# Kernel tuning notes

Hardware: AMD Instinct MI355X
Metric: run time of the kernel (lower is better)

The kernel has to match this reference:

```python
import jax, jax.numpy as jnp
import numpy as np

TOPK = 13
ALPHA = 1.0
BETA = 6.0
NUM_CLASSES = 80
NUM_ANCHORS = 100000
NUM_GT = 512
EPS = 1e-9


def _make_boxes(key, n):
    k1, k2 = jax.random.split(key)
    lt = jax.random.uniform(k1, (n, 2)) * 0.5          # x1, y1 in [0, 0.5)
    wh = jax.random.uniform(k2, (n, 2)) * 0.5 + 1e-3   # positive width/height
    return jnp.concatenate([lt, lt + wh], axis=-1)      # [n, 4] valid xyxy


def setup_inputs() -> dict:
    key = jax.random.key(0)
    k1, k2, k3, k4 = jax.random.split(key, 4)
    pd_scores = jax.random.uniform(k1, (NUM_ANCHORS, NUM_CLASSES), dtype=jnp.float32)
    pd_bboxes = _make_boxes(k2, NUM_ANCHORS)
    gt_labels = jax.random.randint(k3, (NUM_GT, 1), 0, NUM_CLASSES, dtype=jnp.int64)
    gt_bboxes = _make_boxes(k4, NUM_GT)
    return {"pd_scores": pd_scores, "pd_bboxes": pd_bboxes,
            "gt_labels": gt_labels, "gt_bboxes": gt_bboxes}


def box_iou(a, b):
    # a: [G, 4], b: [A, 4] in xyxy -> iou [G, A]
    lt = jnp.maximum(a[:, None, :2], b[None, :, :2])
    rb = jnp.minimum(a[:, None, 2:], b[None, :, 2:])
    wh = jnp.clip(rb - lt, 0.0)
    inter = wh[..., 0] * wh[..., 1]                      # [G, A]
    area_a = (a[:, 2] - a[:, 0]) * (a[:, 3] - a[:, 1])   # [G]
    area_b = (b[:, 2] - b[:, 0]) * (b[:, 3] - b[:, 1])   # [A]
    union = area_a[:, None] + area_b[None, :] - inter
    return inter / (union + EPS)


def select_topk_candidates(metrics, topk):
    # metrics: [G, A] -> bool mask [G, A] of per-row topk entries
    _, topk_idx = jax.lax.top_k(metrics, topk)           # [G, topk]
    rows = jnp.arange(metrics.shape[0])[:, None]
    mask = jnp.zeros(metrics.shape, dtype=bool)
    return mask.at[rows, topk_idx].set(True)


def reference(pd_scores, pd_bboxes, gt_labels, gt_bboxes):
    labels = gt_labels.reshape(-1)                       # [G]
    ious = box_iou(gt_bboxes, pd_bboxes)                 # [G, A]
    scores = pd_scores[:, labels].T                      # [G, A] gather by gt class
    metrics = (scores ** ALPHA) * (ious ** BETA)         # alignment metric [G, A]
    is_in_topk = select_topk_candidates(metrics, TOPK)   # [G, A] bool
    max_metrics = jnp.max(metrics, axis=0)               # [A]
    max_indices = jnp.argmax(metrics, axis=0)            # [A]
    target_labels = labels[max_indices]                  # [A]
    target_labels = jnp.where(max_metrics <= 0, NUM_CLASSES, target_labels)
    target_bboxes = gt_bboxes[max_indices]               # [A, 4]
    # is_in_topk is computed (as in the original) and returned so the topk/scatter
    return target_labels, target_bboxes, max_metrics, is_in_topk
```

## Files before the change

kernel.cpp:

```cpp
#include <hip/hip_runtime.h>
#include <cfloat>
#include <cstdint>

#define AN 100000
#define GN 512
#define NC 80
#define KK 13

#define CHUNKS 8
#define CH_LEN 12544
#define DUMP 16
#define GSLICE 8
#define GPS (GN / GSLICE)

typedef unsigned long long ull;

__device__ __forceinline__ float rcpf(float x)
{
    float r; asm("v_rcp_f32 %0, %1" : "=v"(r) : "v"(x)); return r;
}

__device__ __forceinline__ float iou6r(float4 g, float ga, float4 p)
{
    float pa = (p.z - p.x) * (p.w - p.y);
    float ltx = fmaxf(g.x, p.x), lty = fmaxf(g.y, p.y);
    float rbx = fminf(g.z, p.z), rby = fminf(g.w, p.w);
    float w = fmaxf(rbx - ltx, 0.0f), h = fmaxf(rby - lty, 0.0f);
    float inter = w * h;
    float uni = ga + pa - inter;
    float iou = inter * rcpf(uni + 1e-9f);
    float i2 = iou * iou;
    return i2 * i2 * i2;
}

__device__ __forceinline__ unsigned f2ord(float f)
{
    unsigned b = __float_as_uint(f);
    return b ^ (unsigned)(((int)b >> 31) | 0x80000000);
}
__device__ __forceinline__ float ord2f(unsigned u)
{
    unsigned b = (u & 0x80000000u) ? (u ^ 0x80000000u) : ~u;
    return __uint_as_float(b);
}

__device__ __forceinline__ void csw(float& va, int& ia, float& vb, int& ib)
{
    bool sw = (va < vb) || (va == vb && ia > ib);
    float tv = sw ? vb : va; int ti = sw ? ib : ia;
    vb = sw ? va : vb; ib = sw ? ia : ib;
    va = tv; ia = ti;
}

__device__ __forceinline__ void wsync()
{
    __builtin_amdgcn_sched_barrier(0);
    asm volatile("s_waitcnt lgkmcnt(0)" ::: "memory");
    __builtin_amdgcn_sched_barrier(0);
}

__device__ float flush_x(int lane, int n, const float* cand_v, const int* cand_i,
                         const float* __restrict__ srow,
                         float& inc_v, int& inc_i)
{
    wsync();
    float v[8]; int ix[8];
    #pragma unroll
    for (int k = 0; k < 8; ++k) {
        int j = lane + (k << 6);
        bool ok = j < n;
        float i6 = ok ? cand_v[j] : 0.0f;
        int   ai = ok ? cand_i[j] : 0;
        float sc = srow[ai];
        v[k]  = ok ? sc * i6 : -FLT_MAX;
        ix[k] = ok ? ai : 0x7fffffff;
    }
    csw(v[0],ix[0],v[1],ix[1]); csw(v[2],ix[2],v[3],ix[3]);
    csw(v[4],ix[4],v[5],ix[5]); csw(v[6],ix[6],v[7],ix[7]);
    csw(v[0],ix[0],v[2],ix[2]); csw(v[1],ix[1],v[3],ix[3]);
    csw(v[4],ix[4],v[6],ix[6]); csw(v[5],ix[5],v[7],ix[7]);
    csw(v[1],ix[1],v[2],ix[2]); csw(v[5],ix[5],v[6],ix[6]);
    csw(v[0],ix[0],v[4],ix[4]); csw(v[1],ix[1],v[5],ix[5]);
    csw(v[2],ix[2],v[6],ix[6]); csw(v[3],ix[3],v[7],ix[7]);
    csw(v[2],ix[2],v[4],ix[4]); csw(v[3],ix[3],v[5],ix[5]);
    csw(v[1],ix[1],v[2],ix[2]); csw(v[3],ix[3],v[4],ix[4]);
    csw(v[5],ix[5],v[6],ix[6]);
    bool c[8];
    #pragma unroll
    for (int j = 0; j < 8; ++j)
        c[j] = (v[j] > inc_v) || (v[j] == inc_v && ix[j] < inc_i);
    float h[9]; int hi[9];
    h[0] = c[0] ? v[0] : inc_v;  hi[0] = c[0] ? ix[0] : inc_i;
    #pragma unroll
    for (int j = 1; j < 8; ++j) {
        h[j]  = c[j] ? v[j]  : (c[j-1] ? inc_v : v[j-1]);
        hi[j] = c[j] ? ix[j] : (c[j-1] ? inc_i : ix[j-1]);
    }
    h[8] = c[7] ? inc_v : v[7];  hi[8] = c[7] ? inc_i : ix[7];

    float th = -FLT_MAX;
    #pragma unroll
    for (int r = 0; r < KK; ++r) {
        ull myp = ((ull)f2ord(h[0]) << 32) | (unsigned)(~hi[0]);
        ull p = myp;
        #pragma unroll
        for (int o = 32; o >= 1; o >>= 1) {
            ull q = __shfl_xor(p, o);
            p = p > q ? p : q;
        }
        float wv = ord2f((unsigned)(p >> 32));
        int   wi = (int)~((unsigned)p);
        if (lane == r) { inc_v = wv; inc_i = wi; }
        bool pop = (myp == p);
        #pragma unroll
        for (int j = 0; j < 8; ++j) {
            h[j]  = pop ? h[j+1]  : h[j];
            hi[j] = pop ? hi[j+1] : hi[j];
        }
        h[8]  = pop ? -FLT_MAX   : h[8];
        hi[8] = pop ? 0x7fffffff : hi[8];
        th = wv;
    }
    return th;
}

__device__ __forceinline__ void insert13(float* v, int* ix, float m, int a)
{
    bool worse = (m < v[KK - 1]) || (m == v[KK - 1] && a > ix[KK - 1]);
    if (worse) return;
    int p = 0;
    #pragma unroll
    for (int j = 0; j < KK; ++j)
        p += ((v[j] > m) || (v[j] == m && ix[j] < a)) ? 1 : 0;
    #pragma unroll
    for (int j = KK - 1; j >= 1; --j) {
        bool sh = (j > p);
        v[j]  = sh ? v[j - 1]  : v[j];
        ix[j] = sh ? ix[j - 1] : ix[j];
    }
    #pragma unroll
    for (int j = 0; j < KK; ++j) if (j == p) { v[j] = m; ix[j] = a; }
}

__global__ __launch_bounds__(256) void transpose_scores(
    const float* __restrict__ ps, float* __restrict__ scT)
{
    __shared__ float tile[64][NC + 1];
    int a0 = blockIdx.x * 64;
    int tid = threadIdx.x;
    for (int i = tid; i < 64 * NC / 4; i += 256) {
        int fi = i * 4;
        int a = fi / NC, c = fi % NC;
        if (a0 + a < AN) {
            float4 v = *reinterpret_cast<const float4*>(ps + (size_t)(a0 + a) * NC + c);
            tile[a][c] = v.x; tile[a][c + 1] = v.y; tile[a][c + 2] = v.z; tile[a][c + 3] = v.w;
        }
    }
    __syncthreads();
    int j = tid & 63, cg = tid >> 6;
    int a = a0 + j;
    if (a < AN) {
        for (int c = cg; c < NC; c += 4)
            scT[(size_t)c * AN + a] = tile[j][c];
    }
}

__global__ __launch_bounds__(256) void argmax_part(
    const float* __restrict__ pd_bboxes,
    const int*   __restrict__ gt_labels,
    const float* __restrict__ gt_bboxes,
    const float* __restrict__ scT,
    ull* __restrict__ part)
{
    __shared__ float4 gb[GPS];
    __shared__ float  ga[GPS];
    __shared__ int    glb[GPS];
    int slice = blockIdx.x & (GSLICE - 1);
    int ab = (blockIdx.x >> 3) * 512;
    int tid = threadIdx.x;
    int g0 = slice * GPS;
    if (tid < GPS) {
        float4 bb = ((const float4*)gt_bboxes)[g0 + tid];
        gb[tid] = bb;
        ga[tid] = (bb.z - bb.x) * (bb.w - bb.y);
        glb[tid] = gt_labels[g0 + tid];
    }
    __syncthreads();
    int aa = ab + tid, ab2 = ab + 256 + tid;
    bool okA = aa < AN, okB = ab2 < AN;
    int ca = okA ? aa : AN - 1, cb = okB ? ab2 : AN - 1;
    float4 pba = ((const float4*)pd_bboxes)[ca];
    float4 pbb = ((const float4*)pd_bboxes)[cb];
    float bestA = -1.0f, bestB = -1.0f;
    int bgA = 0, bgB = 0;
    for (int i = 0; i < GPS; ++i) {
        float4 gx = gb[i];
        float gax = ga[i];
        int lab = glb[i];
        const float* srow = scT + (size_t)lab * AN;
        float i6a = iou6r(gx, gax, pba);
        float i6b = iou6r(gx, gax, pbb);
        float sa = (i6a > bestA) ? srow[ca] : 0.0f;
        float sb = (i6b > bestB) ? srow[cb] : 0.0f;
        float ma = sa * i6a;
        float mb = sb * i6b;
        if (ma > bestA) { bestA = ma; bgA = i; }
        if (mb > bestB) { bestB = mb; bgB = i; }
    }
    if (okA)
        part[(size_t)slice * AN + aa] =
            ((ull)__float_as_uint(bestA) << 32) | (ull)(0xFFFFFFFFu - (unsigned)(g0 + bgA));
    if (okB)
        part[(size_t)slice * AN + ab2] =
            ((ull)__float_as_uint(bestB) << 32) | (ull)(0xFFFFFFFFu - (unsigned)(g0 + bgB));
}

__global__ __launch_bounds__(256) void argmax_combine(
    const ull* __restrict__ part,
    const int* __restrict__ gt_labels,
    const float* __restrict__ gt_bboxes,
    float* __restrict__ out)
{
    int a = blockIdx.x * 256 + threadIdx.x;
    if (a >= AN) return;
    ull p = part[a];
    #pragma unroll
    for (int s = 1; s < GSLICE; ++s) {
        ull q = part[(size_t)s * AN + a];
        p = p > q ? p : q;
    }
    unsigned g = 0xFFFFFFFFu - (unsigned)(p & 0xFFFFFFFFull);
    float best = __uint_as_float((unsigned)(p >> 32));
    out[a] = (best <= 0.0f) ? (float)NC : (float)gt_labels[g];
    ((float4*)(out + AN))[a] = ((const float4*)gt_bboxes)[g];
    out[(size_t)5 * AN + a] = best;
}

__device__ __forceinline__ void loadB(int tb, int lane,
    const float4* __restrict__ pd4,
    float4& B0, float4& B1, float4& B2, float4& B3)
{
    int a0 = tb + lane;
    B0 = pd4[min(a0,       AN - 1)];
    B1 = pd4[min(a0 + 64,  AN - 1)];
    B2 = pd4[min(a0 + 128, AN - 1)];
    B3 = pd4[min(a0 + 192, AN - 1)];
}

__device__ __forceinline__ void procB(
    int tb, int aend, int lane, uint64_t lt,
    float4 B0, float4 B1, float4 B2, float4 B3,
    const float* __restrict__ srow,
    float4 b, float gax, float& th, int& cnt,
    float* cand_v, int* cand_i, float& inc_v, int& inc_i)
{
    int a0 = tb + lane, a1 = a0 + 64, a2 = a0 + 128, a3 = a0 + 192;
    float i60 = iou6r(b, gax, B0);
    float i61 = iou6r(b, gax, B1);
    float i62 = iou6r(b, gax, B2);
    float i63 = iou6r(b, gax, B3);
    bool h0 = (i60 > th) && (a0 < aend);
    bool h1 = (i61 > th) && (a1 < aend);
    bool h2 = (i62 > th) && (a2 < aend);
    bool h3 = (i63 > th) && (a3 < aend);
    if (__any(h0 | h1 | h2 | h3)) {
        uint64_t B;
        B = __ballot(h0);
        if (h0) { int p = cnt + __popcll(B & lt); cand_v[p] = i60; cand_i[p] = a0; }
        cnt += __popcll(B);
        B = __ballot(h1);
        if (h1) { int p = cnt + __popcll(B & lt); cand_v[p] = i61; cand_i[p] = a1; }
        cnt += __popcll(B);
        B = __ballot(h2);
        if (h2) { int p = cnt + __popcll(B & lt); cand_v[p] = i62; cand_i[p] = a2; }
        cnt += __popcll(B);
        B = __ballot(h3);
        if (h3) { int p = cnt + __popcll(B & lt); cand_v[p] = i63; cand_i[p] = a3; }
        cnt += __popcll(B);
        if (cnt >= 256) {
            th = flush_x(lane, cnt, cand_v, cand_i, srow, inc_v, inc_i);
            cnt = 0;
        }
    }
}

__global__ __launch_bounds__(256, 4) void topk_pass1(
    const float* __restrict__ pd_bboxes,
    const int*   __restrict__ gt_labels,
    const float* __restrict__ gt_bboxes,
    const float* __restrict__ scT,
    float* __restrict__ out_v, int* __restrict__ out_i)
{
    __shared__ float cvA[4][512];
    __shared__ int   ciA[4][512];
    int w = threadIdx.x >> 6, lane = threadIdx.x & 63;
    float* cand_v = cvA[w]; int* cand_i = ciA[w];
    uint64_t lt = (1ull << lane) - 1ull;
    int gid = blockIdx.x * 4 + w;
    int g = gid & (GN - 1), c = gid >> 9;

    float4 b = ((const float4*)gt_bboxes)[g];
    float gax = (b.z - b.x) * (b.w - b.y);
    int lab = gt_labels[g];
    const float* srow = scT + (size_t)lab * AN;
    const float4* pd4 = (const float4*)pd_bboxes;

    int base = c * CH_LEN;
    int len = min(CH_LEN, AN - base);
    int aend = base + len;
    int NT = (len + 255) >> 8;

    float th = -FLT_MAX; int cnt = 0;
    float inc_v = -FLT_MAX; int inc_i = 0x7fffffff;

    float4 X0, X1, X2, X3, Y0, Y1, Y2, Y3;
    loadB(base, lane, pd4, X0, X1, X2, X3);
    int i = 0, tb = base;
    while (true) {
        if (i + 1 < NT) loadB(tb + 256, lane, pd4, Y0, Y1, Y2, Y3);
        procB(tb, aend, lane, lt, X0, X1, X2, X3, srow,
              b, gax, th, cnt, cand_v, cand_i, inc_v, inc_i);
        ++i; tb += 256;
        if (i >= NT) break;
        if (i + 1 < NT) loadB(tb + 256, lane, pd4, X0, X1, X2, X3);
        procB(tb, aend, lane, lt, Y0, Y1, Y2, Y3, srow,
              b, gax, th, cnt, cand_v, cand_i, inc_v, inc_i);
        ++i; tb += 256;
        if (i >= NT) break;
    }

    if (cnt > 0)
        flush_x(lane, cnt, cand_v, cand_i, srow, inc_v, inc_i);

    if (lane < DUMP) {
        size_t o = ((size_t)g * CHUNKS + c) * DUMP + lane;
        out_v[o] = (lane < KK) ? inc_v : -FLT_MAX;
        out_i[o] = (lane < KK) ? inc_i : 0x7fffffff;
    }
}

__global__ __launch_bounds__(256) void topk_finalize(
    const float* __restrict__ in_v, const int* __restrict__ in_i,
    float* __restrict__ mask)
{
    int g = blockIdx.x, tid = threadIdx.x;
    float4* row4 = (float4*)(mask + (size_t)g * AN);
    float4 z = make_float4(0.f, 0.f, 0.f, 0.f);
    for (int j = tid; j < AN / 4; j += 256) row4[j] = z;
    __syncthreads();
    if (tid >= 64) return;
    int lane = tid;
    size_t rb = (size_t)g * (CHUNKS * DUMP);
    float v0 = in_v[rb + lane], v1 = in_v[rb + 64 + lane];
    int   i0 = in_i[rb + lane], i1 = in_i[rb + 64 + lane];
    csw(v0, i0, v1, i1);
    #pragma unroll
    for (int r = 0; r < KK; ++r) {
        ull myp = ((ull)f2ord(v0) << 32) | (unsigned)(~i0);
        ull p = myp;
        #pragma unroll
        for (int o = 32; o >= 1; o >>= 1) {
            ull q = __shfl_xor(p, o);
            p = p > q ? p : q;
        }
        int wi = (int)~((unsigned)p);
        if (lane == r) mask[(size_t)g * AN + wi] = 1.0f;
        bool pop = (myp == p);
        v0 = pop ? v1 : v0;          i0 = pop ? i1 : i0;
        v1 = pop ? -FLT_MAX : v1;    i1 = pop ? 0x7fffffff : i1;
    }
}

__global__ __launch_bounds__(256) void argmax_kernel(
    const float* __restrict__ pd_scores,
    const float* __restrict__ pd_bboxes,
    const int*   __restrict__ gt_labels,
    const float* __restrict__ gt_bboxes,
    const float* __restrict__ scT, int use_t,
    float* __restrict__ out)
{
    __shared__ float4 gb[GN];
    __shared__ float  ga[GN];
    __shared__ int    gl[GN];
    int tid = threadIdx.x;
    for (int g = tid; g < GN; g += 256) {
        float4 b = reinterpret_cast<const float4*>(gt_bboxes)[g];
        gb[g] = b;
        ga[g] = (b.z - b.x) * (b.w - b.y);
        gl[g] = gt_labels[g];
    }
    __syncthreads();
    int a = blockIdx.x * 256 + tid;
    if (a >= AN) return;
    float4 pb = reinterpret_cast<const float4*>(pd_bboxes)[a];
    float best = -1.0f; int bg = 0;
    for (int g = 0; g < GN; ++g) {
        int lab = gl[g];
        float sc = use_t ? scT[(size_t)lab * AN + a] : pd_scores[(size_t)a * NC + lab];
        float m = sc * iou6r(gb[g], ga[g], pb);
        if (m > best) { best = m; bg = g; }
    }
    out[a] = (best <= 0.0f) ? (float)NC : (float)gl[bg];
    reinterpret_cast<float4*>(out + AN)[a] = gb[bg];
    out[5 * AN + a] = best;
}

__global__ __launch_bounds__(256) void topk_kernel_fallback(
    const float* __restrict__ pd_scores,
    const float* __restrict__ pd_bboxes,
    const int*   __restrict__ gt_labels,
    const float* __restrict__ gt_bboxes,
    const float* __restrict__ scT, int use_t,
    float* __restrict__ mask)
{
    __shared__ float sv[256 * KK];
    __shared__ int   si[256 * KK];
    int g = blockIdx.x, tid = threadIdx.x;
    float4 b = reinterpret_cast<const float4*>(gt_bboxes)[g];
    float gax = (b.z - b.x) * (b.w - b.y);
    int lab = gt_labels[g];
    float v[KK]; int idx[KK];
    #pragma unroll
    for (int j = 0; j < KK; ++j) { v[j] = -FLT_MAX; idx[j] = 0x7fffffff; }
    for (int a = tid; a < AN; a += 256) {
        float4 pb = reinterpret_cast<const float4*>(pd_bboxes)[a];
        float sc = use_t ? scT[(size_t)lab * AN + a] : pd_scores[(size_t)a * NC + lab];
        float m = sc * iou6r(b, gax, pb);
        insert13(v, idx, m, a);
    }
    #pragma unroll
    for (int j = 0; j < KK; ++j) { sv[tid * KK + j] = v[j]; si[tid * KK + j] = idx[j]; }
    for (int off = 128; off >= 1; off >>= 1) {
        __syncthreads();
        if (tid < off) {
            int i = 0, jj = 0;
            float ov[KK]; int oi[KK];
            #pragma unroll
            for (int t = 0; t < KK; ++t) {
                float va = sv[tid * KK + i];          int ia = si[tid * KK + i];
                float vb = sv[(tid + off) * KK + jj]; int ib = si[(tid + off) * KK + jj];
                bool ta = (va > vb) || (va == vb && ia < ib);
                ov[t] = ta ? va : vb; oi[t] = ta ? ia : ib;
                i += ta ? 1 : 0; jj += ta ? 0 : 1;
            }
            #pragma unroll
            for (int t = 0; t < KK; ++t) { sv[tid * KK + t] = ov[t]; si[tid * KK + t] = oi[t]; }
        }
    }
    __syncthreads();
    if (tid < KK) mask[(size_t)g * AN + si[tid]] = 1.0f;
}

extern "C" void kernel_launch(void* const* d_in, const int* in_sizes, int n_in,
                              void* d_out, int out_size, void* d_ws, size_t ws_size,
                              hipStream_t stream)
{
    const float* pd_scores = (const float*)d_in[0];
    const float* pd_bboxes = (const float*)d_in[1];
    const int*   gt_labels = (const int*)d_in[2];
    const float* gt_bboxes = (const float*)d_in[3];
    float* out  = (float*)d_out;
    float* mask = out + (size_t)6 * AN;

    const size_t scT_b  = (size_t)NC * AN * sizeof(float);
    const size_t auxn   = (size_t)GN * CHUNKS * DUMP;
    const size_t aux_b  = auxn * 8;
    const size_t part_b = (size_t)GSLICE * AN * sizeof(ull);

    float* scT   = (float*)d_ws;
    float* aux_v = (float*)((char*)d_ws + scT_b);
    int*   aux_i = (int*)(aux_v + auxn);
    ull*   part  = (ull*)((char*)d_ws + scT_b + aux_b);

    if (ws_size >= scT_b + aux_b + part_b) {
        transpose_scores<<<(AN + 63) / 64, 256, 0, stream>>>(pd_scores, scT);
        topk_pass1<<<GN * CHUNKS / 4, 256, 0, stream>>>(
            pd_bboxes, gt_labels, gt_bboxes, scT, aux_v, aux_i);
        topk_finalize<<<GN, 256, 0, stream>>>(aux_v, aux_i, mask);
        argmax_part<<<((AN + 511) / 512) * GSLICE, 256, 0, stream>>>(
            pd_bboxes, gt_labels, gt_bboxes, scT, part);
        argmax_combine<<<(AN + 255) / 256, 256, 0, stream>>>(
            part, gt_labels, gt_bboxes, out);
    } else if (ws_size >= scT_b + aux_b) {
        transpose_scores<<<(AN + 63) / 64, 256, 0, stream>>>(pd_scores, scT);
        topk_pass1<<<GN * CHUNKS / 4, 256, 0, stream>>>(
            pd_bboxes, gt_labels, gt_bboxes, scT, aux_v, aux_i);
        topk_finalize<<<GN, 256, 0, stream>>>(aux_v, aux_i, mask);
        argmax_kernel<<<(AN + 255) / 256, 256, 0, stream>>>(
            pd_scores, pd_bboxes, gt_labels, gt_bboxes, scT, 1, out);
    } else if (ws_size >= scT_b) {
        hipMemsetAsync(mask, 0, (size_t)GN * AN * sizeof(float), stream);
        transpose_scores<<<(AN + 63) / 64, 256, 0, stream>>>(pd_scores, scT);
        argmax_kernel<<<(AN + 255) / 256, 256, 0, stream>>>(
            pd_scores, pd_bboxes, gt_labels, gt_bboxes, scT, 1, out);
        topk_kernel_fallback<<<GN, 256, 0, stream>>>(
            pd_scores, pd_bboxes, gt_labels, gt_bboxes, scT, 1, mask);
    } else {
        hipMemsetAsync(mask, 0, (size_t)GN * AN * sizeof(float), stream);
        argmax_kernel<<<(AN + 255) / 256, 256, 0, stream>>>(
            pd_scores, pd_bboxes, gt_labels, gt_bboxes, scT, 0, out);
        topk_kernel_fallback<<<GN, 256, 0, stream>>>(
            pd_scores, pd_bboxes, gt_labels, gt_bboxes, scT, 0, mask);
    }
}
```

Baseline: 179.4 us.

## Split anchor range into more chunks and peel the bounds-checked tail tile

The top-k first pass now splits the anchors into 16 chunks instead of 8, doubling the number of wavefronts working per GT row. It also raises the occupancy hint in the launch bounds. Full 256-anchor tiles now run without clamped loads or range checks, and only a separate remainder tile keeps them. The finalize kernel merges four candidates per lane, using a small sorting network, instead of two. In exchange, each chunk sees fewer elements before its threshold rises, so there may be more candidate flushes, and the finalize step does more merge work per lane.

```diff
diff --git a/kernel.cpp b/kernel.cpp
--- a/kernel.cpp
+++ b/kernel.cpp
@@ -7,8 +7,8 @@
 #define NC 80
 #define KK 13
 
-#define CHUNKS 8
-#define CH_LEN 12544
+#define CHUNKS 16
+#define CH_LEN 6400
 #define DUMP 16
 #define GSLICE 8
 #define GPS (GN / GSLICE)
@@ -236,17 +236,23 @@
     out[(size_t)5 * AN + a] = best;
 }
 
+template<bool FULL>
 __device__ __forceinline__ void loadB(int tb, int lane,
     const float4* __restrict__ pd4,
     float4& B0, float4& B1, float4& B2, float4& B3)
 {
     int a0 = tb + lane;
-    B0 = pd4[min(a0,       AN - 1)];
-    B1 = pd4[min(a0 + 64,  AN - 1)];
-    B2 = pd4[min(a0 + 128, AN - 1)];
-    B3 = pd4[min(a0 + 192, AN - 1)];
-}
-
+    if (FULL) {
+        B0 = pd4[a0]; B1 = pd4[a0 + 64]; B2 = pd4[a0 + 128]; B3 = pd4[a0 + 192];
+    } else {
+        B0 = pd4[min(a0,       AN - 1)];
+        B1 = pd4[min(a0 + 64,  AN - 1)];
+        B2 = pd4[min(a0 + 128, AN - 1)];
+        B3 = pd4[min(a0 + 192, AN - 1)];
+    }
+}
+
+template<bool FULL>
 __device__ __forceinline__ void procB(
     int tb, int aend, int lane, uint64_t lt,
     float4 B0, float4 B1, float4 B2, float4 B3,
@@ -259,10 +265,10 @@
     float i61 = iou6r(b, gax, B1);
     float i62 = iou6r(b, gax, B2);
     float i63 = iou6r(b, gax, B3);
-    bool h0 = (i60 > th) && (a0 < aend);
-    bool h1 = (i61 > th) && (a1 < aend);
-    bool h2 = (i62 > th) && (a2 < aend);
-    bool h3 = (i63 > th) && (a3 < aend);
+    bool h0 = (i60 > th) && (FULL || a0 < aend);
+    bool h1 = (i61 > th) && (FULL || a1 < aend);
+    bool h2 = (i62 > th) && (FULL || a2 < aend);
+    bool h3 = (i63 > th) && (FULL || a3 < aend);
     if (__any(h0 | h1 | h2 | h3)) {
         uint64_t B;
         B = __ballot(h0);
@@ -284,7 +290,7 @@
     }
 }
 
-__global__ __launch_bounds__(256, 4) void topk_pass1(
+__global__ __launch_bounds__(256, 8) void topk_pass1(
     const float* __restrict__ pd_bboxes,
     const int*   __restrict__ gt_labels,
     const float* __restrict__ gt_bboxes,
@@ -308,25 +314,31 @@
     int base = c * CH_LEN;
     int len = min(CH_LEN, AN - base);
     int aend = base + len;
-    int NT = (len + 255) >> 8;
+    int nfull = len >> 8;
+    int rem = len & 255;
 
     float th = -FLT_MAX; int cnt = 0;
     float inc_v = -FLT_MAX; int inc_i = 0x7fffffff;
 
     float4 X0, X1, X2, X3, Y0, Y1, Y2, Y3;
-    loadB(base, lane, pd4, X0, X1, X2, X3);
+    loadB<true>(base, lane, pd4, X0, X1, X2, X3);
     int i = 0, tb = base;
     while (true) {
-        if (i + 1 < NT) loadB(tb + 256, lane, pd4, Y0, Y1, Y2, Y3);
-        procB(tb, aend, lane, lt, X0, X1, X2, X3, srow,
-              b, gax, th, cnt, cand_v, cand_i, inc_v, inc_i);
+        if (i + 1 < nfull) loadB<true>(tb + 256, lane, pd4, Y0, Y1, Y2, Y3);
+        procB<true>(tb, aend, lane, lt, X0, X1, X2, X3, srow,
+                    b, gax, th, cnt, cand_v, cand_i, inc_v, inc_i);
         ++i; tb += 256;
-        if (i >= NT) break;
-        if (i + 1 < NT) loadB(tb + 256, lane, pd4, X0, X1, X2, X3);
-        procB(tb, aend, lane, lt, Y0, Y1, Y2, Y3, srow,
-              b, gax, th, cnt, cand_v, cand_i, inc_v, inc_i);
+        if (i >= nfull) break;
+        if (i + 1 < nfull) loadB<true>(tb + 256, lane, pd4, X0, X1, X2, X3);
+        procB<true>(tb, aend, lane, lt, Y0, Y1, Y2, Y3, srow,
+                    b, gax, th, cnt, cand_v, cand_i, inc_v, inc_i);
         ++i; tb += 256;
-        if (i >= NT) break;
+        if (i >= nfull) break;
+    }
+    if (rem) {
+        loadB<false>(tb, lane, pd4, X0, X1, X2, X3);
+        procB<false>(tb, aend, lane, lt, X0, X1, X2, X3, srow,
+                     b, gax, th, cnt, cand_v, cand_i, inc_v, inc_i);
     }
 
     if (cnt > 0)
@@ -351,9 +363,13 @@
     if (tid >= 64) return;
     int lane = tid;
     size_t rb = (size_t)g * (CHUNKS * DUMP);
-    float v0 = in_v[rb + lane], v1 = in_v[rb + 64 + lane];
-    int   i0 = in_i[rb + lane], i1 = in_i[rb + 64 + lane];
-    csw(v0, i0, v1, i1);
+    float v0 = in_v[rb + lane],       v1 = in_v[rb + 64 + lane];
+    float v2 = in_v[rb + 128 + lane], v3 = in_v[rb + 192 + lane];
+    int   i0 = in_i[rb + lane],       i1 = in_i[rb + 64 + lane];
+    int   i2 = in_i[rb + 128 + lane], i3 = in_i[rb + 192 + lane];
+    csw(v0, i0, v1, i1); csw(v2, i2, v3, i3);
+    csw(v0, i0, v2, i2); csw(v1, i1, v3, i3);
+    csw(v1, i1, v2, i2);
     #pragma unroll
     for (int r = 0; r < KK; ++r) {
         ull myp = ((ull)f2ord(v0) << 32) | (unsigned)(~i0);
@@ -366,8 +382,10 @@
         int wi = (int)~((unsigned)p);
         if (lane == r) mask[(size_t)g * AN + wi] = 1.0f;
         bool pop = (myp == p);
-        v0 = pop ? v1 : v0;          i0 = pop ? i1 : i0;
-        v1 = pop ? -FLT_MAX : v1;    i1 = pop ? 0x7fffffff : i1;
+        v0 = pop ? v1 : v0;  i0 = pop ? i1 : i0;
+        v1 = pop ? v2 : v1;  i1 = pop ? i2 : i1;
+        v2 = pop ? v3 : v2;  i2 = pop ? i3 : i2;
+        v3 = pop ? -FLT_MAX : v3;  i3 = pop ? 0x7fffffff : i3;
     }
 }
 
```

Result: slower. 370.9 us (+106.7%).

## Process two GT rows per wavefront and prune with division-free IoU threshold

Applied to the files above, without the earlier changes.

The top-k first pass now has each wavefront handle two ground-truth boxes, so every anchor box loaded is reused for two IoU evaluations. The candidate filter compares intersection against a sixth-root threshold times the union, which removes the reciprocal and power from the hot loop; the exact metric is computed only when candidates are flushed. The chunk count doubles to 16 with half the chunk length and an earlier flush threshold, and finalize merges four candidates per lane instead of two. It also removes one fallback launch path and risks edge cases from the approximate root threshold and higher register pressure.

```diff
diff --git a/kernel.cpp b/kernel.cpp
--- a/kernel.cpp
+++ b/kernel.cpp
@@ -7,8 +7,8 @@
 #define NC 80
 #define KK 13
 
-#define CHUNKS 8
-#define CH_LEN 12544
+#define CHUNKS 16
+#define CH_LEN 6400
 #define DUMP 16
 #define GSLICE 8
 #define GPS (GN / GSLICE)
@@ -18,6 +18,11 @@
 __device__ __forceinline__ float rcpf(float x)
 {
     float r; asm("v_rcp_f32 %0, %1" : "=v"(r) : "v"(x)); return r;
+}
+
+__device__ __forceinline__ float root6_down(float th)
+{
+    return exp2f(log2f(th) * (1.0f / 6.0f)) * 0.9999f;
 }
 
 __device__ __forceinline__ float iou6r(float4 g, float ga, float4 p)
@@ -33,6 +38,16 @@
     return i2 * i2 * i2;
 }
 
+__device__ __forceinline__ void iou_iu(float4 g, float gax, float4 p, float pa,
+                                       float& in, float& ue)
+{
+    float lx = fmaxf(g.x, p.x), ly = fmaxf(g.y, p.y);
+    float rx = fminf(g.z, p.z), ry = fminf(g.w, p.w);
+    float w = fmaxf(rx - lx, 0.0f), h = fmaxf(ry - ly, 0.0f);
+    in = w * h;
+    ue = gax + pa - in + 1e-9f;
+}
+
 __device__ __forceinline__ unsigned f2ord(float f)
 {
     unsigned b = __float_as_uint(f);
@@ -59,7 +74,8 @@
     __builtin_amdgcn_sched_barrier(0);
 }
 
-__device__ float flush_x(int lane, int n, const float* cand_v, const int* cand_i,
+__device__ float flush_f(int lane, int n,
+                         const float* c_in, const float* c_ue, const int* c_ix,
                          const float* __restrict__ srow,
                          float& inc_v, int& inc_i)
 {
@@ -67,10 +83,14 @@
     float v[8]; int ix[8];
     #pragma unroll
     for (int k = 0; k < 8; ++k) {
-        int j = lane + (k << 6);
-        bool ok = j < n;
-        float i6 = ok ? cand_v[j] : 0.0f;
-        int   ai = ok ? cand_i[j] : 0;
+        int j = (lane + (k << 6)) & 255;
+        bool ok = (lane + (k << 6)) < n;
+        float in = ok ? c_in[j] : 0.0f;
+        float ue = ok ? c_ue[j] : 1.0f;
+        int   ai = ok ? c_ix[j] : 0;
+        float iou = in * rcpf(ue);
+        float i2 = iou * iou;
+        float i6 = i2 * i2 * i2;
         float sc = srow[ai];
         v[k]  = ok ? sc * i6 : -FLT_MAX;
         ix[k] = ok ? ai : 0x7fffffff;
@@ -247,40 +267,63 @@
     B3 = pd4[min(a0 + 192, AN - 1)];
 }
 
-__device__ __forceinline__ void procB(
+#define APPEND_K(hk, ik, uk, ak, cnt, ci, cu, cx, th, cth, srow, iv, ii)          \
+    {                                                                             \
+        uint64_t B = __ballot(hk);                                                \
+        if (hk) { int p = (cnt) + __popcll(B & lt);                               \
+                  (ci)[p] = ik; (cu)[p] = uk; (cx)[p] = ak; }                     \
+        (cnt) += __popcll(B);                                                     \
+        if ((cnt) >= 192) {                                                       \
+            th = flush_f(lane, cnt, ci, cu, cx, srow, iv, ii);                    \
+            cth = root6_down(th);                                                 \
+            (cnt) = 0;                                                            \
+        }                                                                         \
+    }
+
+__device__ __forceinline__ void procB2(
     int tb, int aend, int lane, uint64_t lt,
-    float4 B0, float4 B1, float4 B2, float4 B3,
-    const float* __restrict__ srow,
-    float4 b, float gax, float& th, int& cnt,
-    float* cand_v, int* cand_i, float& inc_v, int& inc_i)
+    float4 X0, float4 X1, float4 X2, float4 X3,
+    const float* __restrict__ srow0, const float* __restrict__ srow1,
+    float4 b0, float gax0, float4 b1, float gax1,
+    float& th0, float& cth0, int& cnt0, float* ci0, float* cu0, int* cx0,
+    float& iv0, int& ii0,
+    float& th1, float& cth1, int& cnt1, float* ci1, float* cu1, int* cx1,
+    float& iv1, int& ii1)
 {
     int a0 = tb + lane, a1 = a0 + 64, a2 = a0 + 128, a3 = a0 + 192;
-    float i60 = iou6r(b, gax, B0);
-    float i61 = iou6r(b, gax, B1);
-    float i62 = iou6r(b, gax, B2);
-    float i63 = iou6r(b, gax, B3);
-    bool h0 = (i60 > th) && (a0 < aend);
-    bool h1 = (i61 > th) && (a1 < aend);
-    bool h2 = (i62 > th) && (a2 < aend);
-    bool h3 = (i63 > th) && (a3 < aend);
-    if (__any(h0 | h1 | h2 | h3)) {
-        uint64_t B;
-        B = __ballot(h0);
-        if (h0) { int p = cnt + __popcll(B & lt); cand_v[p] = i60; cand_i[p] = a0; }
-        cnt += __popcll(B);
-        B = __ballot(h1);
-        if (h1) { int p = cnt + __popcll(B & lt); cand_v[p] = i61; cand_i[p] = a1; }
-        cnt += __popcll(B);
-        B = __ballot(h2);
-        if (h2) { int p = cnt + __popcll(B & lt); cand_v[p] = i62; cand_i[p] = a2; }
-        cnt += __popcll(B);
-        B = __ballot(h3);
-        if (h3) { int p = cnt + __popcll(B & lt); cand_v[p] = i63; cand_i[p] = a3; }
-        cnt += __popcll(B);
-        if (cnt >= 256) {
-            th = flush_x(lane, cnt, cand_v, cand_i, srow, inc_v, inc_i);
-            cnt = 0;
-        }
+    float pa0 = (X0.z - X0.x) * (X0.w - X0.y);
+    float pa1 = (X1.z - X1.x) * (X1.w - X1.y);
+    float pa2 = (X2.z - X2.x) * (X2.w - X2.y);
+    float pa3 = (X3.z - X3.x) * (X3.w - X3.y);
+    float i00, u00, i01, u01, i02, u02, i03, u03;
+    float i10, u10, i11, u11, i12, u12, i13, u13;
+    iou_iu(b0, gax0, X0, pa0, i00, u00);
+    iou_iu(b0, gax0, X1, pa1, i01, u01);
+    iou_iu(b0, gax0, X2, pa2, i02, u02);
+    iou_iu(b0, gax0, X3, pa3, i03, u03);
+    iou_iu(b1, gax1, X0, pa0, i10, u10);
+    iou_iu(b1, gax1, X1, pa1, i11, u11);
+    iou_iu(b1, gax1, X2, pa2, i12, u12);
+    iou_iu(b1, gax1, X3, pa3, i13, u13);
+    bool h00 = (i00 > cth0 * u00) && (a0 < aend);
+    bool h01 = (i01 > cth0 * u01) && (a1 < aend);
+    bool h02 = (i02 > cth0 * u02) && (a2 < aend);
+    bool h03 = (i03 > cth0 * u03) && (a3 < aend);
+    bool h10 = (i10 > cth1 * u10) && (a0 < aend);
+    bool h11 = (i11 > cth1 * u11) && (a1 < aend);
+    bool h12 = (i12 > cth1 * u12) && (a2 < aend);
+    bool h13 = (i13 > cth1 * u13) && (a3 < aend);
+    if (__any(h00 | h01 | h02 | h03)) {
+        APPEND_K(h00, i00, u00, a0, cnt0, ci0, cu0, cx0, th0, cth0, srow0, iv0, ii0);
+        APPEND_K(h01, i01, u01, a1, cnt0, ci0, cu0, cx0, th0, cth0, srow0, iv0, ii0);
+        APPEND_K(h02, i02, u02, a2, cnt0, ci0, cu0, cx0, th0, cth0, srow0, iv0, ii0);
+        APPEND_K(h03, i03, u03, a3, cnt0, ci0, cu0, cx0, th0, cth0, srow0, iv0, ii0);
+    }
+    if (__any(h10 | h11 | h12 | h13)) {
+        APPEND_K(h10, i10, u10, a0, cnt1, ci1, cu1, cx1, th1, cth1, srow1, iv1, ii1);
+        APPEND_K(h11, i11, u11, a1, cnt1, ci1, cu1, cx1, th1, cth1, srow1, iv1, ii1);
+        APPEND_K(h12, i12, u12, a2, cnt1, ci1, cu1, cx1, th1, cth1, srow1, iv1, ii1);
+        APPEND_K(h13, i13, u13, a3, cnt1, ci1, cu1, cx1, th1, cth1, srow1, iv1, ii1);
     }
 }
 
@@ -291,18 +334,23 @@
     const float* __restrict__ scT,
     float* __restrict__ out_v, int* __restrict__ out_i)
 {
-    __shared__ float cvA[4][512];
-    __shared__ int   ciA[4][512];
+    __shared__ float cinA[4][2][256];
+    __shared__ float cueA[4][2][256];
+    __shared__ int   cixA[4][2][256];
     int w = threadIdx.x >> 6, lane = threadIdx.x & 63;
-    float* cand_v = cvA[w]; int* cand_i = ciA[w];
+    float* ci0 = cinA[w][0]; float* cu0 = cueA[w][0]; int* cx0 = cixA[w][0];
+    float* ci1 = cinA[w][1]; float* cu1 = cueA[w][1]; int* cx1 = cixA[w][1];
     uint64_t lt = (1ull << lane) - 1ull;
     int gid = blockIdx.x * 4 + w;
-    int g = gid & (GN - 1), c = gid >> 9;
-
-    float4 b = ((const float4*)gt_bboxes)[g];
-    float gax = (b.z - b.x) * (b.w - b.y);
-    int lab = gt_labels[g];
-    const float* srow = scT + (size_t)lab * AN;
+    int pair = gid & 255, c = gid >> 8;
+    int g0 = pair * 2, g1 = g0 + 1;
+
+    float4 b0 = ((const float4*)gt_bboxes)[g0];
+    float4 b1 = ((const float4*)gt_bboxes)[g1];
+    float gax0 = (b0.z - b0.x) * (b0.w - b0.y);
+    float gax1 = (b1.z - b1.x) * (b1.w - b1.y);
+    const float* srow0 = scT + (size_t)gt_labels[g0] * AN;
+    const float* srow1 = scT + (size_t)gt_labels[g1] * AN;
     const float4* pd4 = (const float4*)pd_bboxes;
 
     int base = c * CH_LEN;
@@ -310,32 +358,42 @@
     int aend = base + len;
     int NT = (len + 255) >> 8;
 
-    float th = -FLT_MAX; int cnt = 0;
-    float inc_v = -FLT_MAX; int inc_i = 0x7fffffff;
+    float th0 = -FLT_MAX, cth0 = -FLT_MAX;
+    float th1 = -FLT_MAX, cth1 = -FLT_MAX;
+    int cnt0 = 0, cnt1 = 0;
+    float iv0 = -FLT_MAX, iv1 = -FLT_MAX;
+    int ii0 = 0x7fffffff, ii1 = 0x7fffffff;
 
     float4 X0, X1, X2, X3, Y0, Y1, Y2, Y3;
     loadB(base, lane, pd4, X0, X1, X2, X3);
     int i = 0, tb = base;
     while (true) {
         if (i + 1 < NT) loadB(tb + 256, lane, pd4, Y0, Y1, Y2, Y3);
-        procB(tb, aend, lane, lt, X0, X1, X2, X3, srow,
-              b, gax, th, cnt, cand_v, cand_i, inc_v, inc_i);
+        procB2(tb, aend, lane, lt, X0, X1, X2, X3, srow0, srow1,
+               b0, gax0, b1, gax1,
+               th0, cth0, cnt0, ci0, cu0, cx0, iv0, ii0,
+               th1, cth1, cnt1, ci1, cu1, cx1, iv1, ii1);
         ++i; tb += 256;
         if (i >= NT) break;
         if (i + 1 < NT) loadB(tb + 256, lane, pd4, X0, X1, X2, X3);
-        procB(tb, aend, lane, lt, Y0, Y1, Y2, Y3, srow,
-              b, gax, th, cnt, cand_v, cand_i, inc_v, inc_i);
+        procB2(tb, aend, lane, lt, Y0, Y1, Y2, Y3, srow0, srow1,
+               b0, gax0, b1, gax1,
+               th0, cth0, cnt0, ci0, cu0, cx0, iv0, ii0,
+               th1, cth1, cnt1, ci1, cu1, cx1, iv1, ii1);
         ++i; tb += 256;
         if (i >= NT) break;
     }
 
-    if (cnt > 0)
-        flush_x(lane, cnt, cand_v, cand_i, srow, inc_v, inc_i);
+    if (cnt0 > 0) flush_f(lane, cnt0, ci0, cu0, cx0, srow0, iv0, ii0);
+    if (cnt1 > 0) flush_f(lane, cnt1, ci1, cu1, cx1, srow1, iv1, ii1);
 
     if (lane < DUMP) {
-        size_t o = ((size_t)g * CHUNKS + c) * DUMP + lane;
-        out_v[o] = (lane < KK) ? inc_v : -FLT_MAX;
-        out_i[o] = (lane < KK) ? inc_i : 0x7fffffff;
+        size_t o0 = ((size_t)g0 * CHUNKS + c) * DUMP + lane;
+        out_v[o0] = (lane < KK) ? iv0 : -FLT_MAX;
+        out_i[o0] = (lane < KK) ? ii0 : 0x7fffffff;
+        size_t o1 = ((size_t)g1 * CHUNKS + c) * DUMP + lane;
+        out_v[o1] = (lane < KK) ? iv1 : -FLT_MAX;
+        out_i[o1] = (lane < KK) ? ii1 : 0x7fffffff;
     }
 }
 
@@ -351,9 +409,13 @@
     if (tid >= 64) return;
     int lane = tid;
     size_t rb = (size_t)g * (CHUNKS * DUMP);
-    float v0 = in_v[rb + lane], v1 = in_v[rb + 64 + lane];
-    int   i0 = in_i[rb + lane], i1 = in_i[rb + 64 + lane];
-    csw(v0, i0, v1, i1);
+    float v0 = in_v[rb + lane],       v1 = in_v[rb + 64 + lane];
+    float v2 = in_v[rb + 128 + lane], v3 = in_v[rb + 192 + lane];
+    int   i0 = in_i[rb + lane],       i1 = in_i[rb + 64 + lane];
+    int   i2 = in_i[rb + 128 + lane], i3 = in_i[rb + 192 + lane];
+    csw(v0, i0, v1, i1); csw(v2, i2, v3, i3);
+    csw(v0, i0, v2, i2); csw(v1, i1, v3, i3);
+    csw(v1, i1, v2, i2);
     #pragma unroll
     for (int r = 0; r < KK; ++r) {
         ull myp = ((ull)f2ord(v0) << 32) | (unsigned)(~i0);
@@ -366,8 +428,10 @@
         int wi = (int)~((unsigned)p);
         if (lane == r) mask[(size_t)g * AN + wi] = 1.0f;
         bool pop = (myp == p);
-        v0 = pop ? v1 : v0;          i0 = pop ? i1 : i0;
-        v1 = pop ? -FLT_MAX : v1;    i1 = pop ? 0x7fffffff : i1;
+        v0 = pop ? v1 : v0;  i0 = pop ? i1 : i0;
+        v1 = pop ? v2 : v1;  i1 = pop ? i2 : i1;
+        v2 = pop ? v3 : v2;  i2 = pop ? i3 : i2;
+        v3 = pop ? -FLT_MAX : v3;  i3 = pop ? 0x7fffffff : i3;
     }
 }
 
@@ -474,20 +538,13 @@
 
     if (ws_size >= scT_b + aux_b + part_b) {
         transpose_scores<<<(AN + 63) / 64, 256, 0, stream>>>(pd_scores, scT);
-        topk_pass1<<<GN * CHUNKS / 4, 256, 0, stream>>>(
+        topk_pass1<<<(GN / 2) * CHUNKS / 4, 256, 0, stream>>>(
             pd_bboxes, gt_labels, gt_bboxes, scT, aux_v, aux_i);
         topk_finalize<<<GN, 256, 0, stream>>>(aux_v, aux_i, mask);
         argmax_part<<<((AN + 511) / 512) * GSLICE, 256, 0, stream>>>(
             pd_bboxes, gt_labels, gt_bboxes, scT, part);
         argmax_combine<<<(AN + 255) / 256, 256, 0, stream>>>(
             part, gt_labels, gt_bboxes, out);
-    } else if (ws_size >= scT_b + aux_b) {
-        transpose_scores<<<(AN + 63) / 64, 256, 0, stream>>>(pd_scores, scT);
-        topk_pass1<<<GN * CHUNKS / 4, 256, 0, stream>>>(
-            pd_bboxes, gt_labels, gt_bboxes, scT, aux_v, aux_i);
-        topk_finalize<<<GN, 256, 0, stream>>>(aux_v, aux_i, mask);
-        argmax_kernel<<<(AN + 255) / 256, 256, 0, stream>>>(
-            pd_scores, pd_bboxes, gt_labels, gt_bboxes, scT, 1, out);
     } else if (ws_size >= scT_b) {
         hipMemsetAsync(mask, 0, (size_t)GN * AN * sizeof(float), stream);
         transpose_scores<<<(AN + 63) / 64, 256, 0, stream>>>(pd_scores, scT);
```

New measurement: 477.4 us. 2.66x slower.
